# Kernel optimization log

Hardware: AMD Instinct MI355X
Metric: run time of the kernel (lower is better)

Reference implementation:

```python
import jax, jax.numpy as jnp
import numpy as np

B, T, C = 2, 2048, 1024
NH = 16

def setup_inputs() -> dict:
    key = jax.random.key(0)
    ks = jax.random.split(key, 5)
    s = 0.02
    return {
        "x": jax.random.normal(ks[0], (B, T, C), dtype=jnp.float32),
        "w_attn": jax.random.normal(ks[1], (C, 3 * C), dtype=jnp.float32) * s,
        "b_attn": jax.random.normal(ks[2], (3 * C,), dtype=jnp.float32) * s,
        "w_proj": jax.random.normal(ks[3], (C, C), dtype=jnp.float32) * s,
        "b_proj": jax.random.normal(ks[4], (C,), dtype=jnp.float32) * s,
        "n_heads": NH,
    }

def reference(x, w_attn, b_attn, w_proj, b_proj, n_heads):
    Bx, Tx, Cx = x.shape
    hd = Cx // n_heads
    qkv = x @ w_attn + b_attn                      # [B,T,3C]
    q, k, v = jnp.split(qkv, 3, axis=-1)
    # [B,T,H,hd] -> [B,H,T,hd]
    q = q.reshape(Bx, Tx, n_heads, hd).transpose(0, 2, 1, 3)
    k = k.reshape(Bx, Tx, n_heads, hd).transpose(0, 2, 1, 3)
    v = v.reshape(Bx, Tx, n_heads, hd).transpose(0, 2, 1, 3)
    scale = 1.0 / np.sqrt(hd).astype(np.float32)
    att = jnp.einsum('bhqd,bhkd->bhqk', q, k) * scale   # [B,H,T,T]
    causal = jnp.tril(jnp.ones((Tx, Tx), dtype=bool))
    att = jnp.where(causal[None, None], att, -jnp.inf)
    att = jax.nn.softmax(att, axis=-1)
    y = jnp.einsum('bhqk,bhkd->bhqd', att, v)            # [B,H,T,hd]
    y = y.transpose(0, 2, 1, 3).reshape(Bx, Tx, Cx)
    return y @ w_proj + b_proj
```

## Files before the change

### kernel.cpp

```cpp
#include <hip/hip_runtime.h>

typedef __bf16 bf16x8 __attribute__((ext_vector_type(8)));
typedef __bf16 bf16x4 __attribute__((ext_vector_type(4)));
typedef float  f32x4  __attribute__((ext_vector_type(4)));
typedef float  f32x16 __attribute__((ext_vector_type(16)));
typedef unsigned int u32;

#define MFMA_BF16(a, b, c) __builtin_amdgcn_mfma_f32_16x16x32_bf16((a), (b), (c), 0, 0, 0)
#define MFMA32(a, b, c) __builtin_amdgcn_mfma_f32_32x32x16_bf16((a), (b), (c), 0, 0, 0)
#define NEG_INF (-1e30f)
#define SCL 0.18033688f

__device__ __forceinline__ void gld16(const void* g, void* l) {
  __builtin_amdgcn_global_load_lds(
      (const __attribute__((address_space(1))) void*)g,
      (__attribute__((address_space(3))) void*)l, 16, 0, 0);
}

__global__ void cast_f32_bf16(const float* __restrict__ in,
                              __bf16* __restrict__ out, int n) {
  int i = (blockIdx.x * 256 + threadIdx.x) * 8;
  if (i >= n) return;
  float4 a = *(const float4*)&in[i];
  float4 b = *(const float4*)&in[i + 4];
  bf16x8 v;
  v[0] = (__bf16)a.x; v[1] = (__bf16)a.y; v[2] = (__bf16)a.z; v[3] = (__bf16)a.w;
  v[4] = (__bf16)b.x; v[5] = (__bf16)b.y; v[6] = (__bf16)b.z; v[7] = (__bf16)b.w;
  *(bf16x8*)&out[i] = v;
}

__global__ void transpose_f32_bf16(const float* __restrict__ in,
                                   __bf16* __restrict__ out, int R, int C) {
  __shared__ float t[32][33];
  int tx = threadIdx.x & 31, ty = threadIdx.x >> 5;
  int x = blockIdx.x * 32 + tx;
  int y0 = blockIdx.y * 32 + ty;
#pragma unroll
  for (int i = 0; i < 4; ++i)
    t[ty + 8 * i][tx] = in[(size_t)(y0 + 8 * i) * C + x];
  __syncthreads();
  int x2 = blockIdx.y * 32 + tx;
#pragma unroll
  for (int i = 0; i < 4; ++i)
    out[(size_t)(blockIdx.x * 32 + ty + 8 * i) * R + x2] = (__bf16)t[tx][ty + 8 * i];
}

#define BN 128
#define BK 64

template <int BMT, typename TC>
__global__ __launch_bounds__(256) void gemm_bt_bias(
    const __bf16* __restrict__ A, const __bf16* __restrict__ Bt,
    const float* __restrict__ bias, TC* __restrict__ Cmat,
    int M, int N, int K) {
  constexpr int NI = BMT / 32;
  __shared__ __align__(16) __bf16 As[BMT * BK];
  __shared__ __align__(16) __bf16 Bs[BN * BK];
  int tid = threadIdx.x;
  int wave = tid >> 6, lane = tid & 63;
  int l16 = lane & 15, quad = lane >> 4;
  int wm = wave >> 1, wn = wave & 1;
  int m0 = blockIdx.y * BMT, n0 = blockIdx.x * BN;

  f32x4 acc[NI][4];
#pragma unroll
  for (int i = 0; i < NI; ++i)
#pragma unroll
    for (int j = 0; j < 4; ++j) acc[i][j] = (f32x4){0.f, 0.f, 0.f, 0.f};

  int row = tid >> 3;
  int kc = ((tid & 7) ^ ((tid >> 3) & 7)) * 8;
  int xr = (l16 & 7) * 8;

  for (int k0 = 0; k0 < K; k0 += BK) {
#pragma unroll
    for (int i = 0; i < NI; ++i)
      gld16(&A[(size_t)(m0 + row + i * 32) * K + k0 + kc],
            (char*)As + (i * 256 + wave * 64) * 16);
#pragma unroll
    for (int j = 0; j < 4; ++j)
      gld16(&Bt[(size_t)(n0 + row + j * 32) * K + k0 + kc],
            (char*)Bs + (j * 256 + wave * 64) * 16);
    __syncthreads();
#pragma unroll
    for (int ks = 0; ks < 2; ++ks) {
      bf16x8 af[NI], bfr[4];
#pragma unroll
      for (int i = 0; i < NI; ++i)
        af[i] = *(const bf16x8*)&As[(wm * (BMT / 2) + i * 16 + l16) * BK +
                                    ((ks * 32 + quad * 8) ^ xr)];
#pragma unroll
      for (int j = 0; j < 4; ++j)
        bfr[j] = *(const bf16x8*)&Bs[(wn * 64 + j * 16 + l16) * BK +
                                     ((ks * 32 + quad * 8) ^ xr)];
#pragma unroll
      for (int i = 0; i < NI; ++i)
#pragma unroll
        for (int j = 0; j < 4; ++j) acc[i][j] = MFMA_BF16(af[i], bfr[j], acc[i][j]);
    }
    __syncthreads();
  }
#pragma unroll
  for (int i = 0; i < NI; ++i) {
#pragma unroll
    for (int j = 0; j < 4; ++j) {
      int col = n0 + wn * 64 + j * 16 + l16;
      float bv = bias[col];
#pragma unroll
      for (int r = 0; r < 4; ++r) {
        int rw = m0 + wm * (BMT / 2) + i * 16 + quad * 4 + r;
        Cmat[(size_t)rw * N + col] = (TC)(acc[i][j][r] + bv);
      }
    }
  }
}

#define BARX do { asm volatile("" ::: "memory"); __builtin_amdgcn_s_barrier(); \
                  asm volatile("" ::: "memory"); } while (0)
#define WLGKM do { asm volatile("s_waitcnt lgkmcnt(0)" ::: "memory"); \
                   __builtin_amdgcn_sched_barrier(0); } while (0)
#define WVM4 asm volatile("s_waitcnt vmcnt(4)" ::: "memory")
#define STA8(SBUF, SKS, T) do { \
    gld16(srcA1 + (size_t)(T) * 64 + (SKS) * 32, (char*)&As[SBUF][SKS][0] + tid * 16); \
    gld16(srcA2 + (size_t)(T) * 64 + (SKS) * 32, (char*)&As[SBUF][SKS][0] + tid * 16 + 8192); \
  } while (0)
#define STB8(SBUF, SKS, T) do { \
    gld16(srcB1 + (size_t)(T) * 64 + (SKS) * 32, (char*)&Bs[SBUF][SKS][0] + tid * 16); \
    gld16(srcB2 + (size_t)(T) * 64 + (SKS) * 32, (char*)&Bs[SBUF][SKS][0] + tid * 16 + 8192); \
  } while (0)
#define LDA4(CBUF, CKS, MQ) do { \
    const __bf16* p_ = &As[CBUF][CKS][(wm * 128 + (MQ) * 64 + l16) * 32 + xrd]; \
    af[0] = *(const bf16x8*)(p_);        af[1] = *(const bf16x8*)(p_ + 512); \
    af[2] = *(const bf16x8*)(p_ + 1024); af[3] = *(const bf16x8*)(p_ + 1536); \
  } while (0)
#define LDB3(CBUF, CKS) do { \
    const __bf16* p_ = &Bs[CBUF][CKS][(wn * 48 + l16) * 32 + xrd]; \
    bfr[0] = *(const bf16x8*)(p_);       bfr[1] = *(const bf16x8*)(p_ + 512); \
    bfr[2] = *(const bf16x8*)(p_ + 1024); \
  } while (0)
#define MM12(MQ) do { \
    __builtin_amdgcn_s_setprio(1); \
    _Pragma("unroll") for (int mi_ = 0; mi_ < 4; ++mi_) \
    _Pragma("unroll") for (int nj_ = 0; nj_ < 3; ++nj_) \
      acc[(MQ) * 4 + mi_][nj_] = MFMA_BF16(af[mi_], bfr[nj_], acc[(MQ) * 4 + mi_][nj_]); \
    __builtin_amdgcn_s_setprio(0); \
  } while (0)

__global__ __launch_bounds__(512, 2) void gemm_qkv_8ph(
    const __bf16* __restrict__ A, const __bf16* __restrict__ Bt,
    const float* __restrict__ bias, __bf16* __restrict__ qkv,
    __bf16* __restrict__ vt) {
  constexpr int GK = 1024, GN = 3072, NT = 16;
  __shared__ __align__(16) __bf16 As[2][2][256 * 32];
  __shared__ __align__(16) __bf16 Bs[2][2][256 * 32];
  const int tid = threadIdx.x;
  const int wave = tid >> 6, lane = tid & 63;
  const int l16 = lane & 15, quad = lane >> 4;
  const int wm = wave >> 2, wn = wave & 3;
  const int m0 = blockIdx.y * 256, n0 = blockIdx.x * 192;

  const int row0 = tid >> 2;
  const int kc = (((tid & 3) ^ ((row0 >> 1) & 3)) * 8);
  const int xrd = (quad ^ ((l16 >> 1) & 3)) * 8;

  const __bf16* srcA1 = A + (size_t)(m0 + row0) * GK + kc;
  const __bf16* srcA2 = srcA1 + (size_t)128 * GK;
  const __bf16* srcB1 = Bt + (size_t)(n0 + row0) * GK + kc;
  const int br2 = (row0 + 128 < 192) ? row0 + 128 : 191;
  const __bf16* srcB2 = Bt + (size_t)(n0 + br2) * GK + kc;

  f32x4 acc[8][3];
#pragma unroll
  for (int m = 0; m < 8; ++m)
#pragma unroll
    for (int n = 0; n < 3; ++n) acc[m][n] = (f32x4){0.f, 0.f, 0.f, 0.f};

  STA8(0, 0, 0); STB8(0, 0, 0);
  STA8(0, 1, 0); STB8(0, 1, 0);
  STA8(1, 0, 1); STB8(1, 0, 1);
  WVM4;
  BARX;

  bf16x8 af[4], bfr[3];
#pragma unroll 1
  for (int i = 0; i < NT / 2; ++i) {
    const int v = 2 * i + 1;
    const int t2 = (2 * i + 2 < NT) ? 2 * i + 2 : NT - 1;
    const int t3 = (2 * i + 3 < NT) ? 2 * i + 3 : NT - 1;
    LDA4(0, 0, 0); LDB3(0, 0); STA8(1, 1, v);
    BARX; WLGKM; MM12(0); BARX;
    LDA4(0, 0, 1); STB8(1, 1, v);
    BARX; WLGKM; MM12(1); BARX;
    LDA4(0, 1, 0); LDB3(0, 1); STA8(0, 0, t2);
    BARX; WLGKM; MM12(0); BARX;
    LDA4(0, 1, 1); STB8(0, 0, t2);
    BARX; WLGKM; MM12(1); WVM4; BARX;
    LDA4(1, 0, 0); LDB3(1, 0); STA8(0, 1, t2);
    BARX; WLGKM; MM12(0); BARX;
    LDA4(1, 0, 1); STB8(0, 1, t2);
    BARX; WLGKM; MM12(1); BARX;
    LDA4(1, 1, 0); LDB3(1, 1); STA8(1, 0, t3);
    BARX; WLGKM; MM12(0); BARX;
    LDA4(1, 1, 1); STB8(1, 0, t3);
    BARX; WLGKM; MM12(1); WVM4; BARX;
  }

#pragma unroll
  for (int n = 0; n < 3; ++n) {
    const int c0 = n0 + wn * 48 + n * 16;
    const int col = c0 + l16;
    const float bv = bias[col];
    if (c0 < 2048) {
#pragma unroll
      for (int m = 0; m < 8; ++m) {
        const int rw = m0 + wm * 128 + m * 16 + quad * 4;
#pragma unroll
        for (int r = 0; r < 4; ++r)
          qkv[(size_t)(rw + r) * GN + col] = (__bf16)(acc[m][n][r] + bv);
      }
    } else {
      const int h = (col - 2048) >> 6, d = col & 63;
#pragma unroll
      for (int m = 0; m < 8; ++m) {
        const int t0 = m0 + wm * 128 + m * 16 + quad * 4;
        const int b = t0 >> 11, tt = t0 & 2047;
        bf16x4 pb;
#pragma unroll
        for (int r = 0; r < 4; ++r) pb[r] = (__bf16)(acc[m][n][r] + bv);
        *(bf16x4*)&vt[(size_t)((b * 16 + h) * 64 + d) * 2048 + tt] = pb;
      }
    }
  }
}

#define CVTPK(D, LO, HI) \
  asm("v_cvt_pk_bf16_f32 %0, %1, %2" : "=v"(D) : "v"(LO), "v"(HI))
#define SWAP32(DST, SRC) \
  asm("v_permlane32_swap_b32 %0, %1" : "+v"(DST), "+v"(SRC))

__device__ __forceinline__ bf16x8 mk8(u32 a, u32 b, u32 c, u32 d) {
  union { u32 u[4]; bf16x8 h; } x;
  x.u[0] = a; x.u[1] = b; x.u[2] = c; x.u[3] = d;
  return x.h;
}

__global__ __launch_bounds__(128, 3) void attn_causal(
    const __bf16* __restrict__ qkv, const __bf16* __restrict__ vt,
    __bf16* __restrict__ y) {
  __shared__ __align__(16) __bf16 Kb[2][64 * 64];
  __shared__ __align__(16) __bf16 Vb[2][64 * 64];
  const int tid = threadIdx.x;
  const int wave = tid >> 6, lane = tid & 63;
  const int l32 = lane & 31, hi = lane >> 5;
  const int bh = blockIdx.x;
  const int b = bh >> 4, h = bh & 15;
  const int RS = 3072;
  const int qt = 31 - (int)blockIdx.y;

  const int row8 = tid >> 3;
  const int kcs = ((tid & 7) ^ (row8 & 7)) * 8;
  const __bf16* kbase = qkv + (size_t)(b * 2048) * RS + 1024 + h * 64 + kcs;
  const __bf16* vbase = vt + (size_t)(bh * 64) * 2048 + kcs;

  const __bf16* qp = qkv + (size_t)(b * 2048 + qt * 64 + wave * 32 + l32) * RS +
                     h * 64 + hi * 8;
  bf16x8 qf[4];
#pragma unroll
  for (int kc = 0; kc < 4; ++kc) qf[kc] = *(const bf16x8*)(qp + kc * 16);

  float l4[4] = {0.f, 0.f, 0.f, 0.f};
  f32x16 o0, o1;
#pragma unroll
  for (int r = 0; r < 16; ++r) { o0[r] = 0.f; o1[r] = 0.f; }

#pragma unroll
  for (int i = 0; i < 4; ++i) {
    gld16(kbase + (size_t)(i * 16 + row8) * RS, (char*)Kb[0] + (i * 128 + tid) * 16);
    gld16(vbase + (size_t)(i * 16 + row8) * 2048, (char*)Vb[0] + (i * 128 + tid) * 16);
  }
  __syncthreads();

  const int xr7 = l32 & 7;
  for (int kt = 0; kt <= qt; ++kt) {
    const int cur = kt & 1;
    if (kt < qt) {
#pragma unroll
      for (int i = 0; i < 4; ++i) {
        gld16(kbase + (size_t)((kt + 1) * 64 + i * 16 + row8) * RS,
              (char*)Kb[cur ^ 1] + (i * 128 + tid) * 16);
        gld16(vbase + (size_t)(i * 16 + row8) * 2048 + (kt + 1) * 64,
              (char*)Vb[cur ^ 1] + (i * 128 + tid) * 16);
      }
    }

    f32x16 c0, c1;
#pragma unroll
    for (int r = 0; r < 16; ++r) { c0[r] = 0.f; c1[r] = 0.f; }
    __builtin_amdgcn_s_setprio(1);
#pragma unroll
    for (int kc = 0; kc < 4; ++kc) {
      const int sw = ((kc * 2 + hi) ^ xr7) << 3;
      bf16x8 kf0 = *(const bf16x8*)&Kb[cur][l32 * 64 + sw];
      bf16x8 kf1 = *(const bf16x8*)&Kb[cur][(32 + l32) * 64 + sw];
      c0 = MFMA32(kf0, qf[kc], c0);
      c1 = MFMA32(kf1, qf[kc], c1);
    }
    __builtin_amdgcn_s_setprio(0);

    if (kt == qt) {
      const int qloc = wave * 32 + l32;
#pragma unroll
      for (int r = 0; r < 16; ++r) {
        const int kl = (r & 3) + 8 * (r >> 2) + 4 * hi;
        if (kl > qloc) c0[r] = NEG_INF;
        if (32 + kl > qloc) c1[r] = NEG_INF;
      }
    }

    bf16x8 pb[4];
#pragma unroll
    for (int kb = 0; kb < 2; ++kb) {
      float pv[16];
#pragma unroll
      for (int r = 0; r < 16; ++r) {
        const float sv = (kb ? c1[r] : c0[r]);
        pv[r] = __builtin_amdgcn_exp2f(sv * SCL);
        l4[r & 3] += pv[r];
      }
      u32 a0, a1, b0, b1;
      CVTPK(a0, pv[0], pv[1]);   CVTPK(a1, pv[2], pv[3]);
      CVTPK(b0, pv[4], pv[5]);   CVTPK(b1, pv[6], pv[7]);
      SWAP32(a0, b0); SWAP32(a1, b1);
      pb[kb * 2 + 0] = mk8(a0, a1, b0, b1);
      CVTPK(a0, pv[8], pv[9]);   CVTPK(a1, pv[10], pv[11]);
      CVTPK(b0, pv[12], pv[13]); CVTPK(b1, pv[14], pv[15]);
      SWAP32(a0, b0); SWAP32(a1, b1);
      pb[kb * 2 + 1] = mk8(a0, a1, b0, b1);
    }

    __builtin_amdgcn_s_setprio(1);
#pragma unroll
    for (int kc = 0; kc < 4; ++kc) {
      const int sw = ((kc * 2 + hi) ^ xr7) << 3;
      bf16x8 vf0 = *(const bf16x8*)&Vb[cur][l32 * 64 + sw];
      bf16x8 vf1 = *(const bf16x8*)&Vb[cur][(32 + l32) * 64 + sw];
      o0 = MFMA32(vf0, pb[kc], o0);
      o1 = MFMA32(vf1, pb[kc], o1);
    }
    __builtin_amdgcn_s_setprio(0);
    __syncthreads();
  }

  float lred = (l4[0] + l4[1]) + (l4[2] + l4[3]);
  lred += __shfl_xor(lred, 32);
  const float inv = 1.f / lred;

  const int orow = b * 2048 + qt * 64 + wave * 32 + l32;
  __bf16* yb = y + (size_t)orow * 1024 + h * 64 + hi * 4;
#pragma unroll
  for (int db = 0; db < 2; ++db) {
#pragma unroll
    for (int g = 0; g < 4; ++g) {
      bf16x4 w;
#pragma unroll
      for (int j = 0; j < 4; ++j)
        w[j] = (__bf16)((db ? o1[g * 4 + j] : o0[g * 4 + j]) * inv);
      *(bf16x4*)&yb[db * 32 + g * 8] = w;
    }
  }
}

extern "C" void kernel_launch(void* const* d_in, const int* in_sizes, int n_in,
                              void* d_out, int out_size, void* d_ws, size_t ws_size,
                              hipStream_t stream) {
  (void)in_sizes; (void)n_in; (void)out_size; (void)ws_size;
  const float* x      = (const float*)d_in[0];
  const float* w_attn = (const float*)d_in[1];
  const float* b_attn = (const float*)d_in[2];
  const float* w_proj = (const float*)d_in[3];
  const float* b_proj = (const float*)d_in[4];
  float* out = (float*)d_out;

  __bf16* wt_attn = (__bf16*)d_ws;
  __bf16* wt_proj = wt_attn + (size_t)3072 * 1024;
  __bf16* qkv     = wt_proj + (size_t)1024 * 1024;
  __bf16* ybuf    = qkv + (size_t)4096 * 3072;
  __bf16* vtbuf   = ybuf + (size_t)4096 * 1024;

  cast_f32_bf16<<<4096 * 1024 / 2048, 256, 0, stream>>>(x, ybuf, 4096 * 1024);

  transpose_f32_bf16<<<dim3(3072 / 32, 1024 / 32), 256, 0, stream>>>(w_attn, wt_attn, 1024, 3072);
  transpose_f32_bf16<<<dim3(1024 / 32, 1024 / 32), 256, 0, stream>>>(w_proj, wt_proj, 1024, 1024);

  gemm_qkv_8ph<<<dim3(3072 / 192, 4096 / 256), 512, 0, stream>>>(
      ybuf, wt_attn, b_attn, qkv, vtbuf);

  attn_causal<<<dim3(32, 32), 128, 0, stream>>>(qkv, vtbuf, ybuf);

  gemm_bt_bias<64, float><<<dim3(1024 / BN, 4096 / 64), 256, 0, stream>>>(
      ybuf, wt_proj, b_proj, out, 4096, 1024, 1024);
}
```

Before: 184.7 us.

## Split attention KV tiles across wave pairs and pair causal q-tiles per block

The causal attention kernel now uses 256 threads per block, with two wave pairs that each process alternating 64-key tiles (a split-K over the KV sequence). Each block handles two query tiles, p and 31-p, so every block does the same amount of causal work. Partial outputs and row sums from the second KV half are reduced through shared memory that reuses the V buffer. This aims to improve load balance and per-CU parallelism, at the cost of double the LDS footprint, an extra reduction step with barriers, and idle waves on odd-length tails.

```diff
diff --git a/kernel.cpp b/kernel.cpp
--- a/kernel.cpp
+++ b/kernel.cpp
@@ -244,129 +244,164 @@
   return x.h;
 }
 
-__global__ __launch_bounds__(128, 3) void attn_causal(
+__global__ __launch_bounds__(256, 2) void attn_causal(
     const __bf16* __restrict__ qkv, const __bf16* __restrict__ vt,
     __bf16* __restrict__ y) {
-  __shared__ __align__(16) __bf16 Kb[2][64 * 64];
-  __shared__ __align__(16) __bf16 Vb[2][64 * 64];
+  __shared__ __align__(16) __bf16 Kb[2][2][64 * 64];
+  __shared__ __align__(16) __bf16 Vb[2][2][64 * 64];
   const int tid = threadIdx.x;
   const int wave = tid >> 6, lane = tid & 63;
   const int l32 = lane & 31, hi = lane >> 5;
+  const int qh = wave >> 1, kh = wave & 1;
   const int bh = blockIdx.x;
   const int b = bh >> 4, h = bh & 15;
   const int RS = 3072;
-  const int qt = 31 - (int)blockIdx.y;
+  const int p = (int)blockIdx.y;
 
   const int row8 = tid >> 3;
-  const int kcs = ((tid & 7) ^ (row8 & 7)) * 8;
+  const int kcs = (((tid & 7) ^ (row8 & 7) ^ ((row8 >> 3) & 3)) * 8);
   const __bf16* kbase = qkv + (size_t)(b * 2048) * RS + 1024 + h * 64 + kcs;
   const __bf16* vbase = vt + (size_t)(bh * 64) * 2048 + kcs;
-
-  const __bf16* qp = qkv + (size_t)(b * 2048 + qt * 64 + wave * 32 + l32) * RS +
-                     h * 64 + hi * 8;
-  bf16x8 qf[4];
-#pragma unroll
-  for (int kc = 0; kc < 4; ++kc) qf[kc] = *(const bf16x8*)(qp + kc * 16);
-
-  float l4[4] = {0.f, 0.f, 0.f, 0.f};
-  f32x16 o0, o1;
-#pragma unroll
-  for (int r = 0; r < 16; ++r) { o0[r] = 0.f; o1[r] = 0.f; }
-
-#pragma unroll
-  for (int i = 0; i < 4; ++i) {
-    gld16(kbase + (size_t)(i * 16 + row8) * RS, (char*)Kb[0] + (i * 128 + tid) * 16);
-    gld16(vbase + (size_t)(i * 16 + row8) * 2048, (char*)Vb[0] + (i * 128 + tid) * 16);
-  }
-  __syncthreads();
-
-  const int xr7 = l32 & 7;
-  for (int kt = 0; kt <= qt; ++kt) {
-    const int cur = kt & 1;
-    if (kt < qt) {
-#pragma unroll
-      for (int i = 0; i < 4; ++i) {
-        gld16(kbase + (size_t)((kt + 1) * 64 + i * 16 + row8) * RS,
-              (char*)Kb[cur ^ 1] + (i * 128 + tid) * 16);
-        gld16(vbase + (size_t)(i * 16 + row8) * 2048 + (kt + 1) * 64,
-              (char*)Vb[cur ^ 1] + (i * 128 + tid) * 16);
-      }
-    }
-
-    f32x16 c0, c1;
-#pragma unroll
-    for (int r = 0; r < 16; ++r) { c0[r] = 0.f; c1[r] = 0.f; }
-    __builtin_amdgcn_s_setprio(1);
-#pragma unroll
-    for (int kc = 0; kc < 4; ++kc) {
-      const int sw = ((kc * 2 + hi) ^ xr7) << 3;
-      bf16x8 kf0 = *(const bf16x8*)&Kb[cur][l32 * 64 + sw];
-      bf16x8 kf1 = *(const bf16x8*)&Kb[cur][(32 + l32) * 64 + sw];
-      c0 = MFMA32(kf0, qf[kc], c0);
-      c1 = MFMA32(kf1, qf[kc], c1);
-    }
-    __builtin_amdgcn_s_setprio(0);
-
-    if (kt == qt) {
-      const int qloc = wave * 32 + l32;
+  const int xr = (l32 & 7) ^ ((l32 >> 3) & 3);
+  float* sc = (float*)Vb;
+
+#pragma unroll 1
+  for (int phase = 0; phase < 2; ++phase) {
+    const int qt = phase ? 31 - p : p;
+    const int nit = (qt + 2) >> 1;
+
+    const __bf16* qp = qkv +
+        (size_t)(b * 2048 + qt * 64 + qh * 32 + l32) * RS + h * 64 + hi * 8;
+    bf16x8 qf[4];
+#pragma unroll
+    for (int kc = 0; kc < 4; ++kc) qf[kc] = *(const bf16x8*)(qp + kc * 16);
+
+    float l4[4] = {0.f, 0.f, 0.f, 0.f};
+    f32x16 o0, o1;
+#pragma unroll
+    for (int r = 0; r < 16; ++r) { o0[r] = 0.f; o1[r] = 0.f; }
+
+#pragma unroll
+    for (int s = 0; s < 2; ++s)
+#pragma unroll
+      for (int i = 0; i < 2; ++i) {
+        gld16(kbase + (size_t)(s * 64 + i * 32 + row8) * RS,
+              (char*)Kb[0][s] + (i * 256 + tid) * 16);
+        gld16(vbase + (size_t)(i * 32 + row8) * 2048 + s * 64,
+              (char*)Vb[0][s] + (i * 256 + tid) * 16);
+      }
+    __syncthreads();
+
+    for (int it = 0; it < nit; ++it) {
+      const int cur = it & 1;
+      if (it + 1 < nit) {
+        const int kb2 = (it + 1) * 128;
+#pragma unroll
+        for (int s = 0; s < 2; ++s)
+#pragma unroll
+          for (int i = 0; i < 2; ++i) {
+            gld16(kbase + (size_t)(kb2 + s * 64 + i * 32 + row8) * RS,
+                  (char*)Kb[cur ^ 1][s] + (i * 256 + tid) * 16);
+            gld16(vbase + (size_t)(i * 32 + row8) * 2048 + kb2 + s * 64,
+                  (char*)Vb[cur ^ 1][s] + (i * 256 + tid) * 16);
+          }
+      }
+
+      const int ktile = 2 * it + kh;
+      if (ktile <= qt) {
+        f32x16 c0, c1;
+#pragma unroll
+        for (int r = 0; r < 16; ++r) { c0[r] = 0.f; c1[r] = 0.f; }
+        __builtin_amdgcn_s_setprio(1);
+#pragma unroll
+        for (int kc = 0; kc < 4; ++kc) {
+          const int sw = ((kc * 2 + hi) ^ xr) << 3;
+          bf16x8 kf0 = *(const bf16x8*)&Kb[cur][kh][l32 * 64 + sw];
+          bf16x8 kf1 = *(const bf16x8*)&Kb[cur][kh][(32 + l32) * 64 + sw];
+          c0 = MFMA32(kf0, qf[kc], c0);
+          c1 = MFMA32(kf1, qf[kc], c1);
+        }
+        __builtin_amdgcn_s_setprio(0);
+
+        if (ktile == qt) {
+          const int qloc = qh * 32 + l32;
+#pragma unroll
+          for (int r = 0; r < 16; ++r) {
+            const int kl = (r & 3) + 8 * (r >> 2) + 4 * hi;
+            if (kl > qloc) c0[r] = NEG_INF;
+            if (32 + kl > qloc) c1[r] = NEG_INF;
+          }
+        }
+
+        bf16x8 pb[4];
+#pragma unroll
+        for (int kb = 0; kb < 2; ++kb) {
+          float pv[16];
+#pragma unroll
+          for (int r = 0; r < 16; ++r) {
+            const float sv = (kb ? c1[r] : c0[r]);
+            pv[r] = __builtin_amdgcn_exp2f(sv * SCL);
+            l4[r & 3] += pv[r];
+          }
+          u32 a0, a1, b0, b1;
+          CVTPK(a0, pv[0], pv[1]);   CVTPK(a1, pv[2], pv[3]);
+          CVTPK(b0, pv[4], pv[5]);   CVTPK(b1, pv[6], pv[7]);
+          SWAP32(a0, b0); SWAP32(a1, b1);
+          pb[kb * 2 + 0] = mk8(a0, a1, b0, b1);
+          CVTPK(a0, pv[8], pv[9]);   CVTPK(a1, pv[10], pv[11]);
+          CVTPK(b0, pv[12], pv[13]); CVTPK(b1, pv[14], pv[15]);
+          SWAP32(a0, b0); SWAP32(a1, b1);
+          pb[kb * 2 + 1] = mk8(a0, a1, b0, b1);
+        }
+
+        __builtin_amdgcn_s_setprio(1);
+#pragma unroll
+        for (int kc = 0; kc < 4; ++kc) {
+          const int sw = ((kc * 2 + hi) ^ xr) << 3;
+          bf16x8 vf0 = *(const bf16x8*)&Vb[cur][kh][l32 * 64 + sw];
+          bf16x8 vf1 = *(const bf16x8*)&Vb[cur][kh][(32 + l32) * 64 + sw];
+          o0 = MFMA32(vf0, pb[kc], o0);
+          o1 = MFMA32(vf1, pb[kc], o1);
+        }
+        __builtin_amdgcn_s_setprio(0);
+      }
+      __syncthreads();
+    }
+
+    float lred = (l4[0] + l4[1]) + (l4[2] + l4[3]);
+    lred += __shfl_xor(lred, 32);
+    if (kh == 1) {
+      float* ob = sc + qh * 2048;
 #pragma unroll
       for (int r = 0; r < 16; ++r) {
-        const int kl = (r & 3) + 8 * (r >> 2) + 4 * hi;
-        if (kl > qloc) c0[r] = NEG_INF;
-        if (32 + kl > qloc) c1[r] = NEG_INF;
-      }
-    }
-
-    bf16x8 pb[4];
-#pragma unroll
-    for (int kb = 0; kb < 2; ++kb) {
-      float pv[16];
-#pragma unroll
-      for (int r = 0; r < 16; ++r) {
-        const float sv = (kb ? c1[r] : c0[r]);
-        pv[r] = __builtin_amdgcn_exp2f(sv * SCL);
-        l4[r & 3] += pv[r];
-      }
-      u32 a0, a1, b0, b1;
-      CVTPK(a0, pv[0], pv[1]);   CVTPK(a1, pv[2], pv[3]);
-      CVTPK(b0, pv[4], pv[5]);   CVTPK(b1, pv[6], pv[7]);
-      SWAP32(a0, b0); SWAP32(a1, b1);
-      pb[kb * 2 + 0] = mk8(a0, a1, b0, b1);
-      CVTPK(a0, pv[8], pv[9]);   CVTPK(a1, pv[10], pv[11]);
-      CVTPK(b0, pv[12], pv[13]); CVTPK(b1, pv[14], pv[15]);
-      SWAP32(a0, b0); SWAP32(a1, b1);
-      pb[kb * 2 + 1] = mk8(a0, a1, b0, b1);
-    }
-
-    __builtin_amdgcn_s_setprio(1);
-#pragma unroll
-    for (int kc = 0; kc < 4; ++kc) {
-      const int sw = ((kc * 2 + hi) ^ xr7) << 3;
-      bf16x8 vf0 = *(const bf16x8*)&Vb[cur][l32 * 64 + sw];
-      bf16x8 vf1 = *(const bf16x8*)&Vb[cur][(32 + l32) * 64 + sw];
-      o0 = MFMA32(vf0, pb[kc], o0);
-      o1 = MFMA32(vf1, pb[kc], o1);
-    }
-    __builtin_amdgcn_s_setprio(0);
+        ob[r * 64 + lane] = o0[r];
+        ob[1024 + r * 64 + lane] = o1[r];
+      }
+      if (lane < 32) sc[4096 + qh * 32 + lane] = lred;
+    }
     __syncthreads();
-  }
-
-  float lred = (l4[0] + l4[1]) + (l4[2] + l4[3]);
-  lred += __shfl_xor(lred, 32);
-  const float inv = 1.f / lred;
-
-  const int orow = b * 2048 + qt * 64 + wave * 32 + l32;
-  __bf16* yb = y + (size_t)orow * 1024 + h * 64 + hi * 4;
-#pragma unroll
-  for (int db = 0; db < 2; ++db) {
-#pragma unroll
-    for (int g = 0; g < 4; ++g) {
-      bf16x4 w;
-#pragma unroll
-      for (int j = 0; j < 4; ++j)
-        w[j] = (__bf16)((db ? o1[g * 4 + j] : o0[g * 4 + j]) * inv);
-      *(bf16x4*)&yb[db * 32 + g * 8] = w;
-    }
+    if (kh == 0) {
+      const float* ob = sc + qh * 2048;
+      lred += sc[4096 + qh * 32 + l32];
+      const float inv = 1.f / lred;
+      const int orow = b * 2048 + qt * 64 + qh * 32 + l32;
+      __bf16* yb = y + (size_t)orow * 1024 + h * 64 + hi * 4;
+#pragma unroll
+      for (int db = 0; db < 2; ++db) {
+#pragma unroll
+        for (int g = 0; g < 4; ++g) {
+          bf16x4 w;
+#pragma unroll
+          for (int j = 0; j < 4; ++j) {
+            const float v = (db ? o1[g * 4 + j] : o0[g * 4 + j]) +
+                            ob[db * 1024 + (g * 4 + j) * 64 + lane];
+            w[j] = (__bf16)(v * inv);
+          }
+          *(bf16x4*)&yb[db * 32 + g * 8] = w;
+        }
+      }
+    }
+    __syncthreads();
   }
 }
 
@@ -395,7 +430,7 @@
   gemm_qkv_8ph<<<dim3(3072 / 192, 4096 / 256), 512, 0, stream>>>(
       ybuf, wt_attn, b_attn, qkv, vtbuf);
 
-  attn_causal<<<dim3(32, 32), 128, 0, stream>>>(qkv, vtbuf, ybuf);
+  attn_causal<<<dim3(32, 16), 256, 0, stream>>>(qkv, vtbuf, ybuf);
 
   gemm_bt_bias<64, float><<<dim3(1024 / BN, 4096 / 64), 256, 0, stream>>>(
       ybuf, wt_proj, b_proj, out, 4096, 1024, 1024);
```

Measured after the change: 174.8 us. -5.4%, faster.
